# Kernel optimization log

Hardware: AMD Instinct MI355X
Metric: run time of the kernel (lower is better)

## Reference

```python
import jax, jax.numpy as jnp
import numpy as np

B, N_IN, N_OUT, N_BATCH, N_CONT = 1024, 64, 4096, 64, 16


def setup_inputs() -> dict:
    key = jax.random.key(0)
    ks = jax.random.split(key, 9)
    return {
        "z": jax.random.normal(ks[0], (B, N_IN), dtype=jnp.float32),
        "batch_covariate": jax.random.randint(ks[1], (B,), 0, N_BATCH, dtype=jnp.int32),
        "size_factor": jax.random.uniform(ks[2], (B, 1), dtype=jnp.float32) * 10.0 + 0.1,
        "continuous_covariates": jax.random.normal(ks[3], (B, N_CONT), dtype=jnp.float32),
        "amat_W": jax.random.normal(ks[4], (N_IN, N_OUT), dtype=jnp.float32) * 0.02,
        "embed_A": jax.random.normal(ks[5], (N_BATCH, N_OUT * N_IN), dtype=jnp.float32) * 0.1,
        "embed_h3": jax.random.normal(ks[6], (N_BATCH, N_OUT), dtype=jnp.float32) * 0.1,
        "cont_W": jax.random.normal(ks[7], (N_CONT, N_OUT), dtype=jnp.float32) * 0.02,
        "px_r": jax.random.normal(ks[8], (N_OUT,), dtype=jnp.float32),
    }


def reference(z, batch_covariate, size_factor, continuous_covariates,
              amat_W, embed_A, embed_h3, cont_W, px_r):
    idx = batch_covariate.astype(jnp.int32).reshape(-1)  # [B]
    # h1: Dense(n_out, no bias)
    h1 = z @ amat_W                                      # [B, n_out]
    # dropout deterministic (eval) -> identity; stop_gradient per original
    z_drop = jax.lax.stop_gradient(z)
    # per-sample embedding gather reshaped to [B, n_out, n_in], matvec with z
    A_b = embed_A[idx].reshape(idx.shape[0], N_OUT, N_IN)
    h2 = jnp.einsum("cgl,cl->cg", A_b, z_drop)           # [B, n_out]
    h3 = embed_h3[idx]                                   # [B, n_out]
    h = h1 + h2 + h3 + continuous_covariates @ cont_W
    mu = jax.nn.softmax(h, axis=-1)
    mean = mu * size_factor                              # NB mean
    inverse_dispersion = jnp.exp(px_r)                   # NB inverse dispersion
    return mean, inverse_dispersion
```

## Files before the change

### kernel.cpp

```cpp
#include <hip/hip_runtime.h>
#include <hip/hip_bf16.h>

#define B_SZ   1024
#define NIN    64
#define NOUT   4096
#define NBATCH 64
#define NCONT  16
#define KTOT   96
#define PCAP   48

#define WTB_UNITS  (256 * 3 * 64)
#define XT_ELEMS   (B_SZ * KTOT)
#define WTB_BLOCKS (WTB_UNITS / 256)
#define XT_BLOCKS  (XT_ELEMS / 256)

typedef __attribute__((ext_vector_type(8))) short short8;
typedef __attribute__((ext_vector_type(4))) float f32x4;

__device__ __forceinline__ short f2bf(float f) {
    unsigned u = __float_as_uint(f);
    return (short)((u + 0x7FFFu + ((u >> 16) & 1u)) >> 16);
}
__device__ __forceinline__ short8 pk8(float4 a, float4 b) {
    short8 r;
    r[0]=f2bf(a.x); r[1]=f2bf(a.y); r[2]=f2bf(a.z); r[3]=f2bf(a.w);
    r[4]=f2bf(b.x); r[5]=f2bf(b.y); r[6]=f2bf(b.z); r[7]=f2bf(b.w);
    return r;
}
__device__ __forceinline__ int kpi(int kq, int j) {
    return (j < 4) ? (kq * 4 + j) : (16 + kq * 4 + (j - 4));
}

__global__ __launch_bounds__(256) void k_prep(
    const float* __restrict__ z, const int* __restrict__ idx,
    const float* __restrict__ cont, const float* __restrict__ amat_W,
    const float* __restrict__ cont_W,
    int* __restrict__ cnt_ws, int* __restrict__ perm_ws,
    unsigned short* __restrict__ Xt, unsigned short* __restrict__ Wtb)
{
    const int bid = blockIdx.x, tid = threadIdx.x;

    if (bid < WTB_BLOCKS) {
        const int u   = bid * 256 + tid;
        const int nt  = u / 192, rem = u - nt * 192;
        const int ks  = rem >> 6, lane = rem & 63;
        const int kq  = lane >> 4, nl = lane & 15;
        const int n   = nt * 16 + nl;
        unsigned short v8[8];
        #pragma unroll
        for (int j = 0; j < 8; ++j) {
            const int k = ks * 32 + kpi(kq, j);
            float v = 0.f;
            if (k < NIN)              v = amat_W[k * NOUT + n];
            else if (k < NIN + NCONT) v = cont_W[(k - NIN) * NOUT + n];
            v8[j] = (unsigned short)f2bf(v);
        }
        *(int4*)(Wtb + (size_t)u * 8) = *(int4*)v8;
    } else if (bid < WTB_BLOCKS + XT_BLOCKS) {
        const int i = (bid - WTB_BLOCKS) * 256 + tid;
        const int c = i / KTOT, k = i - c * KTOT;
        float v = 0.f;
        if (k < NIN)              v = z[c * NIN + k];
        else if (k < NIN + NCONT) v = cont[c * NCONT + (k - NIN)];
        Xt[i] = (unsigned short)f2bf(v);
    } else {
        __shared__ int lcnt[NBATCH];
        if (tid < NBATCH) lcnt[tid] = 0;
        for (int i = tid; i < NBATCH * PCAP; i += 256) perm_ws[i] = 0;
        __syncthreads();
        for (int c = tid; c < B_SZ; c += 256) {
            const int b = idx[c];
            const int p = atomicAdd(&lcnt[b], 1);
            if (p < PCAP) perm_ws[b * PCAP + p] = c;
        }
        __syncthreads();
        if (tid < NBATCH) cnt_ws[tid] = min(lcnt[tid], PCAP);
    }
}

__global__ __launch_bounds__(256) void k_xa(
    const unsigned short* __restrict__ Xt, const int* __restrict__ perm_ws,
    unsigned short* __restrict__ Xa)
{
    const int t = blockIdx.x * 256 + threadIdx.x;
    const int u = t >> 6, lane = t & 63;
    const int b = u / 9, r = u - b * 9;
    const int mt = r / 3, ks = r - mt * 3;
    const int kq = lane >> 4, ml = lane & 15;
    const int c = perm_ws[b * PCAP + mt * 16 + ml];
    const unsigned short* s0 = Xt + c * KTOT + ks * 32 + kq * 4;
    ushort4 lo = *(const ushort4*)s0;
    ushort4 hi = *(const ushort4*)(s0 + 16);
    unsigned short v8[8] = {lo.x, lo.y, lo.z, lo.w, hi.x, hi.y, hi.z, hi.w};
    *(int4*)(Xa + (size_t)u * 512 + lane * 8) = *(int4*)v8;
}

__global__ __launch_bounds__(64) void k_gemm(
    const float* __restrict__ embed_A,
    const float* __restrict__ embed_h3,
    const unsigned short* __restrict__ Xa,
    const unsigned short* __restrict__ Wtb,
    const int* __restrict__ cnt_ws,
    const int* __restrict__ perm_ws,
    float* __restrict__ out)
{
    const int lane = threadIdx.x;
    const int nl = lane & 15, kq = lane >> 4;
    const int ib = blockIdx.x;
    const int b  = blockIdx.y;
    const int cnt = cnt_ws[b];
    if (cnt == 0) return;
    const int ntiles = (cnt + 15) >> 4;
    const int t0 = ib * 4;

    const unsigned oxa0 = (unsigned)(b * 9216 + lane * 16);
    const unsigned oxa1 = oxa0 + 3072;
    const unsigned opv  = (unsigned)(b * (PCAP * 4) + kq * 16);
    const unsigned oe0  = (unsigned)((unsigned)(b * NOUT + t0 * 16 + nl) * 256
                                     + kq * 16);
    const unsigned ow0  = (unsigned)(t0 * 3072 + lane * 16);
    const unsigned oh0  = (unsigned)((b * NOUT + t0 * 16 + nl) * 4);

    int4 A00, A01, A02, A10, A11, A12, PV0, PV1;
    asm volatile(
        "global_load_dwordx4 %[a00], %[oxa0], %[xq]\n\t"
        "global_load_dwordx4 %[a01], %[oxa0], %[xq] offset:1024\n\t"
        "global_load_dwordx4 %[a02], %[oxa0], %[xq] offset:2048\n\t"
        "global_load_dwordx4 %[a10], %[oxa1], %[xq]\n\t"
        "global_load_dwordx4 %[a11], %[oxa1], %[xq] offset:1024\n\t"
        "global_load_dwordx4 %[a12], %[oxa1], %[xq] offset:2048\n\t"
        "global_load_dwordx4 %[pv0], %[opv], %[pm]\n\t"
        "global_load_dwordx4 %[pv1], %[opv], %[pm] offset:64\n\t"
        "s_waitcnt vmcnt(0)"
        : [a00]"=&v"(A00), [a01]"=&v"(A01), [a02]"=&v"(A02),
          [a10]"=&v"(A10), [a11]"=&v"(A11), [a12]"=&v"(A12),
          [pv0]"=&v"(PV0), [pv1]"=&v"(PV1)
        : [oxa0]"v"(oxa0), [oxa1]"v"(oxa1), [opv]"v"(opv),
          [xq]"s"(Xa), [pm]"s"(perm_ws)
        : "memory");
    __builtin_amdgcn_sched_barrier(0);

    const short8 az00 = *(const short8*)&A00;
    const short8 az01 = *(const short8*)&A01;
    const short8 az02 = *(const short8*)&A02;
    const short8 az10 = *(const short8*)&A10;
    const short8 az11 = *(const short8*)&A11;
    const short8 az12 = *(const short8*)&A12;

    #pragma unroll
    for (int it = 0; it < 4; ++it) {
        const unsigned oe = oe0 + (unsigned)(it * 4096);
        const unsigned ow = ow0 + (unsigned)(it * 3072);
        const unsigned oh = oh0 + (unsigned)(it * 64);
        const int n = (t0 + it) * 16 + nl;

        int4 E0, E1, E2, E3, W0, W1, W2;
        float H3;
        asm volatile(
            "global_load_dwordx4 %[e0], %[oe], %[ep]\n\t"
            "global_load_dwordx4 %[e1], %[oe], %[ep] offset:64\n\t"
            "global_load_dwordx4 %[e2], %[oe], %[ep] offset:128\n\t"
            "global_load_dwordx4 %[e3], %[oe], %[ep] offset:192\n\t"
            "global_load_dwordx4 %[w0], %[ow], %[wq]\n\t"
            "global_load_dwordx4 %[w1], %[ow], %[wq] offset:1024\n\t"
            "global_load_dwordx4 %[w2], %[ow], %[wq] offset:2048\n\t"
            "global_load_dword   %[h],  %[oh], %[hp]\n\t"
            "s_waitcnt vmcnt(0)"
            : [e0]"=&v"(E0), [e1]"=&v"(E1), [e2]"=&v"(E2), [e3]"=&v"(E3),
              [w0]"=&v"(W0), [w1]"=&v"(W1), [w2]"=&v"(W2), [h]"=&v"(H3)
            : [oe]"v"(oe), [ow]"v"(ow), [oh]"v"(oh),
              [ep]"s"(embed_A), [wq]"s"(Wtb), [hp]"s"(embed_h3)
            : "memory");
        __builtin_amdgcn_sched_barrier(0);

        const short8 eb0 = pk8(*(const float4*)&E0, *(const float4*)&E1);
        const short8 eb1 = pk8(*(const float4*)&E2, *(const float4*)&E3);
        const short8 wt0 = *(const short8*)&W0;
        const short8 wt1 = *(const short8*)&W1;
        const short8 wt2 = *(const short8*)&W2;

        {
            f32x4 acc = {0, 0, 0, 0};
            acc = __builtin_amdgcn_mfma_f32_16x16x32_bf16(az00, eb0, acc, 0, 0, 0);
            acc = __builtin_amdgcn_mfma_f32_16x16x32_bf16(az01, eb1, acc, 0, 0, 0);
            acc = __builtin_amdgcn_mfma_f32_16x16x32_bf16(az00, wt0, acc, 0, 0, 0);
            acc = __builtin_amdgcn_mfma_f32_16x16x32_bf16(az01, wt1, acc, 0, 0, 0);
            acc = __builtin_amdgcn_mfma_f32_16x16x32_bf16(az02, wt2, acc, 0, 0, 0);
            const int sb = kq * 4;
            if (sb + 0 < cnt) out[(size_t)PV0.x * NOUT + n] = acc[0] + H3;
            if (sb + 1 < cnt) out[(size_t)PV0.y * NOUT + n] = acc[1] + H3;
            if (sb + 2 < cnt) out[(size_t)PV0.z * NOUT + n] = acc[2] + H3;
            if (sb + 3 < cnt) out[(size_t)PV0.w * NOUT + n] = acc[3] + H3;
        }
        if (ntiles > 1) {
            f32x4 acc = {0, 0, 0, 0};
            acc = __builtin_amdgcn_mfma_f32_16x16x32_bf16(az10, eb0, acc, 0, 0, 0);
            acc = __builtin_amdgcn_mfma_f32_16x16x32_bf16(az11, eb1, acc, 0, 0, 0);
            acc = __builtin_amdgcn_mfma_f32_16x16x32_bf16(az10, wt0, acc, 0, 0, 0);
            acc = __builtin_amdgcn_mfma_f32_16x16x32_bf16(az11, wt1, acc, 0, 0, 0);
            acc = __builtin_amdgcn_mfma_f32_16x16x32_bf16(az12, wt2, acc, 0, 0, 0);
            const int sb = 16 + kq * 4;
            if (sb + 0 < cnt) out[(size_t)PV1.x * NOUT + n] = acc[0] + H3;
            if (sb + 1 < cnt) out[(size_t)PV1.y * NOUT + n] = acc[1] + H3;
            if (sb + 2 < cnt) out[(size_t)PV1.z * NOUT + n] = acc[2] + H3;
            if (sb + 3 < cnt) out[(size_t)PV1.w * NOUT + n] = acc[3] + H3;
        }
        if (ntiles > 2) {
            const unsigned short* xa2 = Xa + ((size_t)(b * 9 + 6)) * 512 + lane * 8;
            const short8 az20 = *(const short8*)(xa2);
            const short8 az21 = *(const short8*)(xa2 + 512);
            const short8 az22 = *(const short8*)(xa2 + 1024);
            const int4 pv2 = *(const int4*)(perm_ws + b * PCAP + 32 + kq * 4);
            f32x4 acc = {0, 0, 0, 0};
            acc = __builtin_amdgcn_mfma_f32_16x16x32_bf16(az20, eb0, acc, 0, 0, 0);
            acc = __builtin_amdgcn_mfma_f32_16x16x32_bf16(az21, eb1, acc, 0, 0, 0);
            acc = __builtin_amdgcn_mfma_f32_16x16x32_bf16(az20, wt0, acc, 0, 0, 0);
            acc = __builtin_amdgcn_mfma_f32_16x16x32_bf16(az21, wt1, acc, 0, 0, 0);
            acc = __builtin_amdgcn_mfma_f32_16x16x32_bf16(az22, wt2, acc, 0, 0, 0);
            const int sb = 32 + kq * 4;
            if (sb + 0 < cnt) out[(size_t)pv2.x * NOUT + n] = acc[0] + H3;
            if (sb + 1 < cnt) out[(size_t)pv2.y * NOUT + n] = acc[1] + H3;
            if (sb + 2 < cnt) out[(size_t)pv2.z * NOUT + n] = acc[2] + H3;
            if (sb + 3 < cnt) out[(size_t)pv2.w * NOUT + n] = acc[3] + H3;
        }
    }
}

__global__ __launch_bounds__(256) void k_softmax(
    float*       __restrict__ out,
    const float* __restrict__ sf,
    const float* __restrict__ px_r)
{
    const int c   = blockIdx.x;
    const int tid = threadIdx.x;
    float4* row4 = reinterpret_cast<float4*>(out + (size_t)c * NOUT);

    float4 v[4];
    #pragma unroll
    for (int j = 0; j < 4; ++j) v[j] = row4[j * 256 + tid];

    float m = -3.4e38f;
    #pragma unroll
    for (int j = 0; j < 4; ++j)
        m = fmaxf(fmaxf(fmaxf(m, v[j].x), fmaxf(v[j].y, v[j].z)), v[j].w);

    #pragma unroll
    for (int off = 32; off > 0; off >>= 1)
        m = fmaxf(m, __shfl_xor(m, off, 64));

    __shared__ float s_red[8];
    const int wave = tid >> 6;
    const int lane = tid & 63;
    if (lane == 0) s_red[wave] = m;
    __syncthreads();
    m = fmaxf(fmaxf(s_red[0], s_red[1]), fmaxf(s_red[2], s_red[3]));

    float s = 0.f;
    #pragma unroll
    for (int j = 0; j < 4; ++j) {
        v[j].x = __expf(v[j].x - m); v[j].y = __expf(v[j].y - m);
        v[j].z = __expf(v[j].z - m); v[j].w = __expf(v[j].w - m);
        s += v[j].x + v[j].y + v[j].z + v[j].w;
    }
    #pragma unroll
    for (int off = 32; off > 0; off >>= 1)
        s += __shfl_xor(s, off, 64);
    if (lane == 0) s_red[4 + wave] = s;
    __syncthreads();
    s = s_red[4] + s_red[5] + s_red[6] + s_red[7];

    const float scale = sf[c] / s;
    #pragma unroll
    for (int j = 0; j < 4; ++j) {
        v[j].x *= scale; v[j].y *= scale; v[j].z *= scale; v[j].w *= scale;
        row4[j * 256 + tid] = v[j];
    }

    if (c < NOUT / 256) {
        const int i = c * 256 + tid;
        out[(size_t)B_SZ * NOUT + i] = __expf(px_r[i]);
    }
}

extern "C" void kernel_launch(void* const* d_in, const int* in_sizes, int n_in,
                              void* d_out, int out_size, void* d_ws, size_t ws_size,
                              hipStream_t stream)
{
    const float* z       = (const float*)d_in[0];
    const int*   idx     = (const int*)  d_in[1];
    const float* sf      = (const float*)d_in[2];
    const float* cont    = (const float*)d_in[3];
    const float* amat_W  = (const float*)d_in[4];
    const float* embed_A = (const float*)d_in[5];
    const float* eh3     = (const float*)d_in[6];
    const float* cont_W  = (const float*)d_in[7];
    const float* px_r    = (const float*)d_in[8];
    float* out = (float*)d_out;

    char* ws = (char*)d_ws;
    int*            cnt_ws  = (int*)ws;
    int*            perm_ws = (int*)(ws + 256);
    unsigned short* Xt      = (unsigned short*)(ws + 16384);
    unsigned short* Wtb     = (unsigned short*)(ws + 212992);
    unsigned short* Xa      = (unsigned short*)(ws + 999424);

    k_prep<<<WTB_BLOCKS + XT_BLOCKS + 1, 256, 0, stream>>>(
        z, idx, cont, amat_W, cont_W, cnt_ws, perm_ws, Xt, Wtb);

    k_xa<<<144, 256, 0, stream>>>(Xt, perm_ws, Xa);

    dim3 grid1(64, NBATCH);
    k_gemm<<<grid1, 64, 0, stream>>>(embed_A, eh3, Xa, Wtb,
                                     cnt_ws, perm_ws, out);

    k_softmax<<<B_SZ, 256, 0, stream>>>(out, sf, px_r);
}
```

Measured before the change: 36.26 us.

## Gather and convert z/cont rows inside GEMM, drop Xt/Xa staging kernels

Removes the Xt conversion pass in k_prep and the separate k_xa gather kernel. The GEMM kernel now reads the permuted sample rows of z and the continuous covariates directly as fp32 and packs them to bf16 in registers. This saves one kernel launch and two workspace round trips. In exchange, each GEMM block redundantly re-reads and converts its batch's rows with uncoalesced gathers, and the hand-scheduled asm prefetch is replaced by ordinary compiler loads.

```diff
diff --git a/kernel.cpp b/kernel.cpp
--- a/kernel.cpp
+++ b/kernel.cpp
@@ -10,9 +10,7 @@
 #define PCAP   48
 
 #define WTB_UNITS  (256 * 3 * 64)
-#define XT_ELEMS   (B_SZ * KTOT)
 #define WTB_BLOCKS (WTB_UNITS / 256)
-#define XT_BLOCKS  (XT_ELEMS / 256)
 
 typedef __attribute__((ext_vector_type(8))) short short8;
 typedef __attribute__((ext_vector_type(4))) float f32x4;
@@ -36,7 +34,7 @@
     const float* __restrict__ cont, const float* __restrict__ amat_W,
     const float* __restrict__ cont_W,
     int* __restrict__ cnt_ws, int* __restrict__ perm_ws,
-    unsigned short* __restrict__ Xt, unsigned short* __restrict__ Wtb)
+    unsigned short* __restrict__ Wtb)
 {
     const int bid = blockIdx.x, tid = threadIdx.x;
 
@@ -56,13 +54,6 @@
             v8[j] = (unsigned short)f2bf(v);
         }
         *(int4*)(Wtb + (size_t)u * 8) = *(int4*)v8;
-    } else if (bid < WTB_BLOCKS + XT_BLOCKS) {
-        const int i = (bid - WTB_BLOCKS) * 256 + tid;
-        const int c = i / KTOT, k = i - c * KTOT;
-        float v = 0.f;
-        if (k < NIN)              v = z[c * NIN + k];
-        else if (k < NIN + NCONT) v = cont[c * NCONT + (k - NIN)];
-        Xt[i] = (unsigned short)f2bf(v);
     } else {
         __shared__ int lcnt[NBATCH];
         if (tid < NBATCH) lcnt[tid] = 0;
@@ -78,27 +69,11 @@
     }
 }
 
-__global__ __launch_bounds__(256) void k_xa(
-    const unsigned short* __restrict__ Xt, const int* __restrict__ perm_ws,
-    unsigned short* __restrict__ Xa)
-{
-    const int t = blockIdx.x * 256 + threadIdx.x;
-    const int u = t >> 6, lane = t & 63;
-    const int b = u / 9, r = u - b * 9;
-    const int mt = r / 3, ks = r - mt * 3;
-    const int kq = lane >> 4, ml = lane & 15;
-    const int c = perm_ws[b * PCAP + mt * 16 + ml];
-    const unsigned short* s0 = Xt + c * KTOT + ks * 32 + kq * 4;
-    ushort4 lo = *(const ushort4*)s0;
-    ushort4 hi = *(const ushort4*)(s0 + 16);
-    unsigned short v8[8] = {lo.x, lo.y, lo.z, lo.w, hi.x, hi.y, hi.z, hi.w};
-    *(int4*)(Xa + (size_t)u * 512 + lane * 8) = *(int4*)v8;
-}
-
 __global__ __launch_bounds__(64) void k_gemm(
+    const float* __restrict__ z,
+    const float* __restrict__ cont,
     const float* __restrict__ embed_A,
     const float* __restrict__ embed_h3,
-    const unsigned short* __restrict__ Xa,
     const unsigned short* __restrict__ Wtb,
     const int* __restrict__ cnt_ws,
     const int* __restrict__ perm_ws,
@@ -113,39 +88,27 @@
     const int ntiles = (cnt + 15) >> 4;
     const int t0 = ib * 4;
 
-    const unsigned oxa0 = (unsigned)(b * 9216 + lane * 16);
-    const unsigned oxa1 = oxa0 + 3072;
-    const unsigned opv  = (unsigned)(b * (PCAP * 4) + kq * 16);
-    const unsigned oe0  = (unsigned)((unsigned)(b * NOUT + t0 * 16 + nl) * 256
-                                     + kq * 16);
-    const unsigned ow0  = (unsigned)(t0 * 3072 + lane * 16);
-    const unsigned oh0  = (unsigned)((b * NOUT + t0 * 16 + nl) * 4);
-
-    int4 A00, A01, A02, A10, A11, A12, PV0, PV1;
-    asm volatile(
-        "global_load_dwordx4 %[a00], %[oxa0], %[xq]\n\t"
-        "global_load_dwordx4 %[a01], %[oxa0], %[xq] offset:1024\n\t"
-        "global_load_dwordx4 %[a02], %[oxa0], %[xq] offset:2048\n\t"
-        "global_load_dwordx4 %[a10], %[oxa1], %[xq]\n\t"
-        "global_load_dwordx4 %[a11], %[oxa1], %[xq] offset:1024\n\t"
-        "global_load_dwordx4 %[a12], %[oxa1], %[xq] offset:2048\n\t"
-        "global_load_dwordx4 %[pv0], %[opv], %[pm]\n\t"
-        "global_load_dwordx4 %[pv1], %[opv], %[pm] offset:64\n\t"
-        "s_waitcnt vmcnt(0)"
-        : [a00]"=&v"(A00), [a01]"=&v"(A01), [a02]"=&v"(A02),
-          [a10]"=&v"(A10), [a11]"=&v"(A11), [a12]"=&v"(A12),
-          [pv0]"=&v"(PV0), [pv1]"=&v"(PV1)
-        : [oxa0]"v"(oxa0), [oxa1]"v"(oxa1), [opv]"v"(opv),
-          [xq]"s"(Xa), [pm]"s"(perm_ws)
-        : "memory");
-    __builtin_amdgcn_sched_barrier(0);
-
-    const short8 az00 = *(const short8*)&A00;
-    const short8 az01 = *(const short8*)&A01;
-    const short8 az02 = *(const short8*)&A02;
-    const short8 az10 = *(const short8*)&A10;
-    const short8 az11 = *(const short8*)&A11;
-    const short8 az12 = *(const short8*)&A12;
+    const int* pbase = perm_ws + b * PCAP;
+    const int c0 = pbase[nl];
+    const int c1 = pbase[16 + nl];
+    const int4 pv0 = *(const int4*)(pbase + kq * 4);
+    const int4 pv1 = *(const int4*)(pbase + 16 + kq * 4);
+
+    const float4* z4 = (const float4*)z;
+    const float4* q4 = (const float4*)cont;
+    const float4 zero4 = {0.f, 0.f, 0.f, 0.f};
+
+    const short8 az00 = pk8(z4[c0 * 16 + kq],      z4[c0 * 16 + 4 + kq]);
+    const short8 az01 = pk8(z4[c0 * 16 + 8 + kq],  z4[c0 * 16 + 12 + kq]);
+    const short8 az02 = pk8(q4[c0 * 4 + kq],       zero4);
+    const short8 az10 = pk8(z4[c1 * 16 + kq],      z4[c1 * 16 + 4 + kq]);
+    const short8 az11 = pk8(z4[c1 * 16 + 8 + kq],  z4[c1 * 16 + 12 + kq]);
+    const short8 az12 = pk8(q4[c1 * 4 + kq],       zero4);
+
+    const unsigned oe0 = (unsigned)((unsigned)(b * NOUT + t0 * 16 + nl) * 256
+                                    + kq * 16);
+    const unsigned ow0 = (unsigned)(t0 * 3072 + lane * 16);
+    const unsigned oh0 = (unsigned)((b * NOUT + t0 * 16 + nl) * 4);
 
     #pragma unroll
     for (int it = 0; it < 4; ++it) {
@@ -187,10 +150,10 @@
             acc = __builtin_amdgcn_mfma_f32_16x16x32_bf16(az01, wt1, acc, 0, 0, 0);
             acc = __builtin_amdgcn_mfma_f32_16x16x32_bf16(az02, wt2, acc, 0, 0, 0);
             const int sb = kq * 4;
-            if (sb + 0 < cnt) out[(size_t)PV0.x * NOUT + n] = acc[0] + H3;
-            if (sb + 1 < cnt) out[(size_t)PV0.y * NOUT + n] = acc[1] + H3;
-            if (sb + 2 < cnt) out[(size_t)PV0.z * NOUT + n] = acc[2] + H3;
-            if (sb + 3 < cnt) out[(size_t)PV0.w * NOUT + n] = acc[3] + H3;
+            if (sb + 0 < cnt) out[(size_t)pv0.x * NOUT + n] = acc[0] + H3;
+            if (sb + 1 < cnt) out[(size_t)pv0.y * NOUT + n] = acc[1] + H3;
+            if (sb + 2 < cnt) out[(size_t)pv0.z * NOUT + n] = acc[2] + H3;
+            if (sb + 3 < cnt) out[(size_t)pv0.w * NOUT + n] = acc[3] + H3;
         }
         if (ntiles > 1) {
             f32x4 acc = {0, 0, 0, 0};
@@ -200,17 +163,17 @@
             acc = __builtin_amdgcn_mfma_f32_16x16x32_bf16(az11, wt1, acc, 0, 0, 0);
             acc = __builtin_amdgcn_mfma_f32_16x16x32_bf16(az12, wt2, acc, 0, 0, 0);
             const int sb = 16 + kq * 4;
-            if (sb + 0 < cnt) out[(size_t)PV1.x * NOUT + n] = acc[0] + H3;
-            if (sb + 1 < cnt) out[(size_t)PV1.y * NOUT + n] = acc[1] + H3;
-            if (sb + 2 < cnt) out[(size_t)PV1.z * NOUT + n] = acc[2] + H3;
-            if (sb + 3 < cnt) out[(size_t)PV1.w * NOUT + n] = acc[3] + H3;
+            if (sb + 0 < cnt) out[(size_t)pv1.x * NOUT + n] = acc[0] + H3;
+            if (sb + 1 < cnt) out[(size_t)pv1.y * NOUT + n] = acc[1] + H3;
+            if (sb + 2 < cnt) out[(size_t)pv1.z * NOUT + n] = acc[2] + H3;
+            if (sb + 3 < cnt) out[(size_t)pv1.w * NOUT + n] = acc[3] + H3;
         }
         if (ntiles > 2) {
-            const unsigned short* xa2 = Xa + ((size_t)(b * 9 + 6)) * 512 + lane * 8;
-            const short8 az20 = *(const short8*)(xa2);
-            const short8 az21 = *(const short8*)(xa2 + 512);
-            const short8 az22 = *(const short8*)(xa2 + 1024);
-            const int4 pv2 = *(const int4*)(perm_ws + b * PCAP + 32 + kq * 4);
+            const int c2 = pbase[32 + nl];
+            const int4 pv2 = *(const int4*)(pbase + 32 + kq * 4);
+            const short8 az20 = pk8(z4[c2 * 16 + kq],     z4[c2 * 16 + 4 + kq]);
+            const short8 az21 = pk8(z4[c2 * 16 + 8 + kq], z4[c2 * 16 + 12 + kq]);
+            const short8 az22 = pk8(q4[c2 * 4 + kq],      zero4);
             f32x4 acc = {0, 0, 0, 0};
             acc = __builtin_amdgcn_mfma_f32_16x16x32_bf16(az20, eb0, acc, 0, 0, 0);
             acc = __builtin_amdgcn_mfma_f32_16x16x32_bf16(az21, eb1, acc, 0, 0, 0);
@@ -300,17 +263,13 @@
     char* ws = (char*)d_ws;
     int*            cnt_ws  = (int*)ws;
     int*            perm_ws = (int*)(ws + 256);
-    unsigned short* Xt      = (unsigned short*)(ws + 16384);
-    unsigned short* Wtb     = (unsigned short*)(ws + 212992);
-    unsigned short* Xa      = (unsigned short*)(ws + 999424);
-
-    k_prep<<<WTB_BLOCKS + XT_BLOCKS + 1, 256, 0, stream>>>(
-        z, idx, cont, amat_W, cont_W, cnt_ws, perm_ws, Xt, Wtb);
-
-    k_xa<<<144, 256, 0, stream>>>(Xt, perm_ws, Xa);
+    unsigned short* Wtb     = (unsigned short*)(ws + 16384);
+
+    k_prep<<<WTB_BLOCKS + 1, 256, 0, stream>>>(
+        z, idx, cont, amat_W, cont_W, cnt_ws, perm_ws, Wtb);
 
     dim3 grid1(64, NBATCH);
-    k_gemm<<<grid1, 64, 0, stream>>>(embed_A, eh3, Xa, Wtb,
+    k_gemm<<<grid1, 64, 0, stream>>>(z, cont, embed_A, eh3, Wtb,
                                      cnt_ws, perm_ws, out);
 
     k_softmax<<<B_SZ, 256, 0, stream>>>(out, sf, px_r);
```

After: 34.87 us, median of 2. 3.8% less time.
